# Performance work log

Hardware: AMD Instinct MI355X
Metric: run time of the kernel (lower is better)

Reference implementation:

```python
import jax, jax.numpy as jnp
import numpy as np

BN_EPS = 1e-5
LEAKY_SLOPE = 0.1


def conv_bn_leaky(x, w, gamma, beta, mean, var, pad):
    # Conv2d(no bias) + BatchNorm2d(inference) + LeakyReLU(0.1), NCHW/OIHW
    y = jax.lax.conv_general_dilated(
        x, w, window_strides=(1, 1), padding=[(pad, pad), (pad, pad)],
        dimension_numbers=("NCHW", "OIHW", "NCHW"))
    scale = gamma / jnp.sqrt(var + BN_EPS)
    shift = beta - mean * scale
    y = y * scale[None, :, None, None] + shift[None, :, None, None]
    return jnp.where(y > 0, y, LEAKY_SLOPE * y)


def reorg(x, s=2):
    # vedanet Reorg: out[b, (a*s+d)*C + c, i, j] = x[b, c, i*s+a, j*s+d]
    B, C, H, W = x.shape
    Ho, Wo = H // s, W // s
    return x.reshape(B, C, Ho, s, Wo, s).transpose(0, 3, 5, 1, 2, 4).reshape(B, s * s * C, Ho, Wo)


def setup_inputs() -> dict:
    key = jax.random.key(0)
    ks = jax.random.split(key, 10)
    B, H, W = 32, 19, 19
    NC, NA = 20, 5
    return {
        "stage6": jax.random.normal(ks[0], (B, 1024, H, W), jnp.float32),
        "stage5": jax.random.normal(ks[1], (B, 512, 2 * H, 2 * W), jnp.float32),
        "w1": jax.random.normal(ks[2], (64, 512, 1, 1), jnp.float32) * 0.05,
        "g1": jnp.ones((64,), jnp.float32),
        "b1": jnp.zeros((64,), jnp.float32),
        "m1": jax.random.normal(ks[3], (64,), jnp.float32) * 0.1,
        "v1": jax.random.uniform(ks[4], (64,), jnp.float32, 0.5, 1.5),
        "w2": jax.random.normal(ks[5], (1024, 1280, 3, 3), jnp.float32) * 0.02,
        "g2": jnp.ones((1024,), jnp.float32),
        "b2": jnp.zeros((1024,), jnp.float32),
        "m2": jax.random.normal(ks[6], (1024,), jnp.float32) * 0.1,
        "v2": jax.random.uniform(ks[7], (1024,), jnp.float32, 0.5, 1.5),
        "meta_state": jax.random.normal(ks[8], (NC, NA * 6, 1025), jnp.float32) * 0.05,
    }


def reference(stage6, stage5, w1, g1, b1, m1, v1, w2, g2, b2, m2, v2, meta_state):
    # layers[0]: 1x1 conv-bn-leaky on stage5, then Reorg(2) -> (B, 256, H, W)
    x = conv_bn_leaky(stage5, w1, g1, b1, m1, v1, pad=0)
    x = reorg(x, 2)
    # layers[1]: 3x3 conv-bn-leaky on concat -> (B, 1024, H, W)
    pre = conv_bn_leaky(jnp.concatenate([x, stage6], axis=1), w2, g2, b2, m2, v2, pad=1)
    # meta_predict: per-class 1x1 conv, batched as one einsum
    cls_w = meta_state[:, :, :-1]   # (NC, NA*6, 1024)
    cls_b = meta_state[:, :, -1]    # (NC, NA*6)
    out = jnp.einsum("bkij,cmk->bcmij", pre, cls_w) + cls_b[None, :, :, None, None]
    B, NC, M = pre.shape[0], meta_state.shape[0], meta_state.shape[1]
    return out.reshape(B * NC, M, pre.shape[2], pre.shape[3])
```

## Files before the change

kernel.cpp:

```cpp
#include <hip/hip_runtime.h>

typedef unsigned short u16;
typedef unsigned int   u32;

typedef __attribute__((ext_vector_type(8))) short bf16x8;
typedef __attribute__((ext_vector_type(4))) float f32x4;

__device__ __forceinline__ u16 f2bf(float f) {
  u32 u = __float_as_uint(f);
  u32 r = (u + 0x7fffu + ((u >> 16) & 1u)) >> 16;
  return (u16)r;
}

__device__ __forceinline__ void async16(const void* g, void* l) {
  __builtin_amdgcn_global_load_lds(
      (const __attribute__((address_space(1))) u32*)g,
      (__attribute__((address_space(3))) u32*)l, 16, 0, 0);
}

__global__ __launch_bounds__(256) void mega_prep_kern(
    const float* __restrict__ stage5, const float* __restrict__ s6,
    const float* __restrict__ w1,
    const float* __restrict__ g1, const float* __restrict__ b1,
    const float* __restrict__ m1, const float* __restrict__ v1,
    const float* __restrict__ w2, const float* __restrict__ g2,
    const float* __restrict__ b2, const float* __restrict__ m2,
    const float* __restrict__ v2, const float* __restrict__ meta,
    u16* __restrict__ in_bf, u16* __restrict__ w2p,
    u16* __restrict__ clsp, float* __restrict__ clsb,
    float* __restrict__ shift2)
{
  __shared__ __align__(16) char smem[8704];
  const int bid = blockIdx.x;
  const int t = threadIdx.x;

  if (bid < 722) {
    float* sc_s = (float*)smem;
    float* sh_s = (float*)(smem + 256);
    char*  aT   = smem + 512;
    char*  bT   = smem + 4608;
    const int w = t >> 6, lane = t & 63;
    if (t < 64) {
      float s = g1[t] * rsqrtf(v1[t] + 1e-5f);
      sc_s[t] = s;
      sh_s[t] = b1[t] - m1[t] * s;
    }
    const int m0 = bid * 64;
    const int pS = t & 63, gS = t >> 6;
    const int mS = m0 + pS;
    const int bS = mS / 1444, hwS = mS - bS * 1444;
    const float* s5 = stage5 + (size_t)bS * (512 * 1444) + hwS;
    const int ocA = t >> 2, icqA = t & 3;
    const float* w1r = w1 + (size_t)ocA * 512 + icqA * 8;
    char* aW = aT + (ocA >> 4) * 1024 + (icqA * 16 + (ocA & 15)) * 16;
    char* bW = bT + pS * 64 + ((gS ^ ((pS >> 1) & 3))) * 16;
    const int bR = (w * 16 + (lane & 15)) * 64 +
                   (((lane >> 4) ^ (((lane & 15) >> 1) & 3))) * 16;
    f32x4 acc[4] = {};
    __syncthreads();
    const float sA = sc_s[ocA];
    for (int kc = 0; kc < 16; ++kc) {
      const int ic0 = kc * 32;
      float a8[8], b8[8];
#pragma unroll
      for (int e = 0; e < 8; ++e) a8[e] = w1r[ic0 + e];
#pragma unroll
      for (int e = 0; e < 8; ++e) b8[e] = s5[(size_t)(ic0 + gS * 8 + e) * 1444];
      __syncthreads();
      uint4 av, bv;
      av.x = (u32)f2bf(a8[0] * sA) | ((u32)f2bf(a8[1] * sA) << 16);
      av.y = (u32)f2bf(a8[2] * sA) | ((u32)f2bf(a8[3] * sA) << 16);
      av.z = (u32)f2bf(a8[4] * sA) | ((u32)f2bf(a8[5] * sA) << 16);
      av.w = (u32)f2bf(a8[6] * sA) | ((u32)f2bf(a8[7] * sA) << 16);
      bv.x = (u32)f2bf(b8[0]) | ((u32)f2bf(b8[1]) << 16);
      bv.y = (u32)f2bf(b8[2]) | ((u32)f2bf(b8[3]) << 16);
      bv.z = (u32)f2bf(b8[4]) | ((u32)f2bf(b8[5]) << 16);
      bv.w = (u32)f2bf(b8[6]) | ((u32)f2bf(b8[7]) << 16);
      *(uint4*)aW = av;
      *(uint4*)bW = bv;
      __syncthreads();
      bf16x8 bfv = *(const bf16x8*)(bT + bR);
#pragma unroll
      for (int i = 0; i < 4; ++i) {
        bf16x8 af = *(const bf16x8*)(aT + i * 1024 + lane * 16);
        acc[i] = __builtin_amdgcn_mfma_f32_16x16x32_bf16(af, bfv, acc[i], 0, 0, 0);
      }
    }
    const int mE = m0 + w * 16 + (lane & 15);
    const int bE = mE / 1444, hwE = mE - bE * 1444;
    const int h = hwE / 38, wq = hwE - h * 38;
    const int ho = h >> 1, wo = wq >> 1, q = ((h & 1) << 1) | (wq & 1);
    u16* dst = in_bf + (((size_t)bE * 21 + 1 + ho) * 21 + 1 + wo) * 1280 + q * 64;
    const int lq = lane >> 4;
#pragma unroll
    for (int i = 0; i < 4; ++i) {
      int oc = i * 16 + lq * 4;
      float v0 = acc[i][0] + sh_s[oc + 0]; v0 = v0 > 0.f ? v0 : 0.1f * v0;
      float v1_ = acc[i][1] + sh_s[oc + 1]; v1_ = v1_ > 0.f ? v1_ : 0.1f * v1_;
      float v2_ = acc[i][2] + sh_s[oc + 2]; v2_ = v2_ > 0.f ? v2_ : 0.1f * v2_;
      float v3 = acc[i][3] + sh_s[oc + 3]; v3 = v3 > 0.f ? v3 : 0.1f * v3;
      u32 lo = (u32)f2bf(v0) | ((u32)f2bf(v1_) << 16);
      u32 hi = (u32)f2bf(v2_) | ((u32)f2bf(v3) << 16);
      u32* dp = (u32*)(dst + oc);
      dp[0] = lo; dp[1] = hi;
    }
    return;
  }

  if (bid < 3794) {
    u16 (*tile)[66] = (u16(*)[66])smem;
    const int sub = bid - 722;
    const int jt = sub % 6, ct = (sub / 6) % 16, b = sub / 96;
    const int ij0 = jt * 64, c0 = ct * 64;
    const int col = t & 63, rr = t >> 6;
#pragma unroll
    for (int r = 0; r < 16; ++r) {
      int cl = r * 4 + rr;
      int ij = ij0 + col;
      float v = 0.f;
      if (ij < 361) v = s6[((size_t)b * 1024 + c0 + cl) * 361 + ij];
      tile[cl][col] = f2bf(v);
    }
    __syncthreads();
#pragma unroll
    for (int r = 0; r < 16; ++r) {
      int ijl = r * 4 + rr;
      int ij = ij0 + ijl;
      if (ij < 361) {
        int i = ij / 19, j = ij - i * 19;
        in_bf[(((size_t)b * 21 + 1 + i) * 21 + 1 + j) * 1280 + 256 + c0 + col] =
            tile[col][ijl];
      }
    }
    return;
  }

  if (bid < 5394) {
    int gi = (bid - 3794) * 256 + t;
    int b = gi / 12800;
    int rem = gi - b * 12800;
    int p = rem / 160, qq = rem - p * 160;
    int row, col;
    if (p < 21)      { row = 0;      col = p; }
    else if (p < 42) { row = 20;     col = p - 21; }
    else if (p < 61) { row = p - 41; col = 0; }
    else             { row = p - 60; col = 20; }
    uint4 z = {0u, 0u, 0u, 0u};
    *(uint4*)(in_bf + (((size_t)b * 21 + row) * 21 + col) * 1280 + qq * 8) = z;
    return;
  }

  if (bid < 7794) {
    int idx = (bid - 5394) * 256 + t;
    int cm = idx >> 10, k = idx & 1023;
    int tile_ = cm >> 7, g = (cm >> 4) & 7, mm = cm & 15;
    int kc = k >> 5, ksub = (k >> 3) & 3, e = k & 7;
    size_t dst = (((size_t)tile_ * 32 + kc) * 8 + g) * 512
                 + (size_t)(ksub * 16 + mm) * 8 + e;
    clsp[dst] = f2bf(meta[(size_t)cm * 1025 + k]);
    if (idx < 600) clsb[idx] = meta[(size_t)idx * 1025 + 1024];
    if (idx < 1024) {
      float sc = g2[idx] * rsqrtf(v2[idx] + 1e-5f);
      shift2[idx] = b2[idx] - m2[idx] * sc;
    }
    return;
  }

  {
    u16* tile = (u16*)smem;
    const int sub = bid - 7794;
    const int icb = sub % 10;
    const int oc = sub / 10;
    const int ic0 = icb * 128;
    const float sc = g2[oc] * rsqrtf(v2[oc] + 1e-5f);
    const float* src = w2 + (size_t)oc * 11520 + (size_t)ic0 * 9;
#pragma unroll
    for (int p = t; p < 1152; p += 256) {
      float v = src[p];
      int ic_l = p / 9;
      int khw = p - ic_l * 9;
      tile[khw * 130 + ic_l] = f2bf(v * sc);
    }
    __syncthreads();
    if (t < 144) {
      int khw = t >> 4, c = (t >> 2) & 3, ksub = t & 3;
      int kc = khw * 40 + icb * 4 + c;
      const u16* s = &tile[khw * 130 + c * 32 + ksub * 8];
      uint4 v;
      v.x = (u32)s[0] | ((u32)s[1] << 16);
      v.y = (u32)s[2] | ((u32)s[3] << 16);
      v.z = (u32)s[4] | ((u32)s[5] << 16);
      v.w = (u32)s[6] | ((u32)s[7] << 16);
      size_t dst = (((size_t)(oc >> 7) * 360 + kc) * 8 + ((oc >> 4) & 7)) * 512
                   + (size_t)(ksub * 16 + (oc & 15)) * 8;
      *(uint4*)(w2p + dst) = v;
    }
  }
}

__global__ __launch_bounds__(256) void conv2_gemm_kern(
    const u16* __restrict__ Wp, const u16* __restrict__ Ig,
    const float* __restrict__ shift2, u16* __restrict__ pre)
{
  __shared__ u16 Wa[128 * 32];
  __shared__ u16 Ib[128 * 32];
  __shared__ float shft[128];
  const int t = threadIdx.x;
  const int w = t >> 6, lane = t & 63;
  const int lin = blockIdx.x + 91 * blockIdx.y;
  const int m0 = (lin >> 3) * 128;
  const int oc0 = (lin & 7) * 128;

  if (t < 128) shft[t] = shift2[oc0 + t];

  const u16* pW0 = Wp + ((size_t)(oc0 >> 7) * 2880 + w) * 512 + lane * 8;

  const int rw = t >> 2;
  const int rpart = ((t & 3) ^ ((t >> 3) & 3)) * 8;
  int mA = m0 + rw;       if (mA > 11551) mA = 11551;
  int mB = m0 + 64 + rw;  if (mB > 11551) mB = 11551;
  int bA = mA / 361, ijA = mA - bA * 361;
  int ohA = ijA / 19, owA = ijA - ohA * 19;
  int bB = mB / 361, ijB = mB - bB * 361;
  int ohB = ijB / 19, owB = ijB - ohB * 19;
  const u16* pI0 = Ig + (size_t)((bA * 21 + ohA) * 21 + owA) * 1280 + rpart;
  const u16* pI1 = Ig + (size_t)((bB * 21 + ohB) * 21 + owB) * 1280 + rpart;

  u16* waS0 = &Wa[w * 512];
  u16* waS1 = &Wa[2048 + w * 512];
  u16* ibS0 = &Ib[w * 512];
  u16* ibS1 = &Ib[2048 + w * 512];

  const int aBase = (w >> 1) * 2048 + lane * 8;
  const int bBase = (w & 1) * 2048 + (lane & 15) * 32 +
                    (((lane >> 4) ^ ((lane >> 1) & 3))) * 8;

  f32x4 acc[4][4] = {};

  for (int khw = 0; khw < 9; ++khw) {
    const int kh = khw / 3, kw = khw - kh * 3;
    const size_t iOffB = (size_t)(kh * 21 + kw) * 1280;
    const size_t wOffB = (size_t)khw * 40 * 4096;
    for (int icc = 0; icc < 40; ++icc) {
      const size_t io = iOffB + (size_t)icc * 32;
      const size_t wo_ = wOffB + (size_t)icc * 4096;
      async16(pW0 + wo_, waS0);
      async16(pW0 + wo_ + 2048, waS1);
      async16(pI0 + io, ibS0);
      async16(pI1 + io, ibS1);
      __syncthreads();
      bf16x8 af[4], bfv[4];
#pragma unroll
      for (int i = 0; i < 4; ++i)
        af[i] = *(const bf16x8*)&Wa[aBase + i * 512];
#pragma unroll
      for (int j = 0; j < 4; ++j)
        bfv[j] = *(const bf16x8*)&Ib[bBase + j * 512];
#pragma unroll
      for (int i = 0; i < 4; ++i)
#pragma unroll
        for (int j = 0; j < 4; ++j)
          acc[i][j] = __builtin_amdgcn_mfma_f32_16x16x32_bf16(
              af[i], bfv[j], acc[i][j], 0, 0, 0);
      __syncthreads();
    }
  }

  const int aRow = (w >> 1) * 64, bRow = (w & 1) * 64;
  const int lq = lane >> 4, lr = lane & 15;
#pragma unroll
  for (int j = 0; j < 4; ++j) {
    int m = m0 + bRow + j * 16 + lr;
    if (m >= 11552) continue;
    u16* prow = pre + (size_t)m * 1024 + oc0;
#pragma unroll
    for (int i = 0; i < 4; ++i) {
      int ocl = aRow + i * 16 + lq * 4;
      float v0 = acc[i][j][0] + shft[ocl + 0]; v0 = v0 > 0.f ? v0 : 0.1f * v0;
      float v1 = acc[i][j][1] + shft[ocl + 1]; v1 = v1 > 0.f ? v1 : 0.1f * v1;
      float v2 = acc[i][j][2] + shft[ocl + 2]; v2 = v2 > 0.f ? v2 : 0.1f * v2;
      float v3 = acc[i][j][3] + shft[ocl + 3]; v3 = v3 > 0.f ? v3 : 0.1f * v3;
      u32 lo = (u32)f2bf(v0) | ((u32)f2bf(v1) << 16);
      u32 hi = (u32)f2bf(v2) | ((u32)f2bf(v3) << 16);
      u32* dp = (u32*)(prow + ocl);
      dp[0] = lo; dp[1] = hi;
    }
  }
}

__global__ __launch_bounds__(256) void einsum_gemm_kern(
    const u16* __restrict__ Ap, const u16* __restrict__ Bg,
    const float* __restrict__ biasg, float* __restrict__ out)
{
  __shared__ u16 Wa[128 * 32];
  __shared__ u16 Ib[128 * 32];
  __shared__ float sbias[128];
  const int t = threadIdx.x;
  const int w = t >> 6, lane = t & 63;
  const int m0 = blockIdx.x * 128;
  const int cm0 = blockIdx.y * 128;
  if (t < 128) { int c = cm0 + t; sbias[t] = (c < 600) ? biasg[c] : 0.f; }

  const u16* pA0 = Ap + ((size_t)(cm0 >> 7) * 256 + w) * 512 + lane * 8;

  const int rw = t >> 2;
  const int rpart = ((t & 3) ^ ((t >> 3) & 3)) * 8;
  int rB0 = m0 + rw;        if (rB0 > 11551) rB0 = 11551;
  int rB1 = m0 + 64 + rw;   if (rB1 > 11551) rB1 = 11551;
  const u16* pB0 = Bg + (size_t)rB0 * 1024 + rpart;
  const u16* pB1 = Bg + (size_t)rB1 * 1024 + rpart;

  u16* waS0 = &Wa[w * 512];
  u16* waS1 = &Wa[2048 + w * 512];
  u16* ibS0 = &Ib[w * 512];
  u16* ibS1 = &Ib[2048 + w * 512];

  const int aBase = (w >> 1) * 2048 + lane * 8;
  const int bBase = (w & 1) * 2048 + (lane & 15) * 32 +
                    (((lane >> 4) ^ ((lane >> 1) & 3))) * 8;

  f32x4 acc[4][4] = {};

  for (int kt = 0; kt < 32; ++kt) {
    const size_t off = (size_t)kt * 32;
    async16(pA0 + (size_t)kt * 4096, waS0);
    async16(pA0 + (size_t)kt * 4096 + 2048, waS1);
    async16(pB0 + off, ibS0);
    async16(pB1 + off, ibS1);
    __syncthreads();
    bf16x8 af[4], bfv[4];
#pragma unroll
    for (int i = 0; i < 4; ++i)
      af[i] = *(const bf16x8*)&Wa[aBase + i * 512];
#pragma unroll
    for (int j = 0; j < 4; ++j)
      bfv[j] = *(const bf16x8*)&Ib[bBase + j * 512];
#pragma unroll
    for (int i = 0; i < 4; ++i)
#pragma unroll
      for (int j = 0; j < 4; ++j)
        acc[i][j] = __builtin_amdgcn_mfma_f32_16x16x32_bf16(
            af[i], bfv[j], acc[i][j], 0, 0, 0);
    __syncthreads();
  }

  const int aRow = (w >> 1) * 64, bRow = (w & 1) * 64;
  const int lq = lane >> 4, lr = lane & 15;
#pragma unroll
  for (int j = 0; j < 4; ++j) {
    int m = m0 + bRow + j * 16 + lr;
    if (m >= 11552) continue;
    int b = m / 361, ij = m - b * 361;
    float* obase = out + (size_t)b * 216600 + ij;
#pragma unroll
    for (int i = 0; i < 4; ++i) {
      int cml = aRow + i * 16 + lq * 4;
#pragma unroll
      for (int r = 0; r < 4; ++r) {
        int cm = cm0 + cml + r;
        if (cm < 600) obase[(size_t)cm * 361] = acc[i][j][r] + sbias[cml + r];
      }
    }
  }
}

extern "C" void kernel_launch(void* const* d_in, const int* in_sizes, int n_in,
                              void* d_out, int out_size, void* d_ws, size_t ws_size,
                              hipStream_t stream)
{
  const float* stage6 = (const float*)d_in[0];
  const float* stage5 = (const float*)d_in[1];
  const float* w1 = (const float*)d_in[2];
  const float* g1 = (const float*)d_in[3];
  const float* b1 = (const float*)d_in[4];
  const float* m1 = (const float*)d_in[5];
  const float* v1 = (const float*)d_in[6];
  const float* w2 = (const float*)d_in[7];
  const float* g2 = (const float*)d_in[8];
  const float* b2 = (const float*)d_in[9];
  const float* m2 = (const float*)d_in[10];
  const float* v2 = (const float*)d_in[11];
  const float* meta = (const float*)d_in[12];
  float* out = (float*)d_out;

  char* ws = (char*)d_ws;
  u16*   in_bf  = (u16*)(ws);
  u16*   w2p    = (u16*)(ws + 36126720);
  u16*   prebf  = (u16*)(ws + 59719680);
  u16*   clsp   = (u16*)(ws + 83378176);
  float* clsb   = (float*)(ws + 84688896);
  float* shift2 = (float*)(ws + 84691456);

  mega_prep_kern<<<18034, 256, 0, stream>>>(
      stage5, stage6, w1, g1, b1, m1, v1, w2, g2, b2, m2, v2, meta,
      in_bf, w2p, clsp, clsb, shift2);
  conv2_gemm_kern<<<dim3(91, 8), 256, 0, stream>>>(w2p, in_bf, shift2, prebf);
  einsum_gemm_kern<<<dim3(91, 5), 256, 0, stream>>>(clsp, prebf, clsb, out);
}
```

Baseline: 602.8 us.

## Rewrite conv2 GEMM with 256x256 tiles, 4-stage async LDS pipeline, 512 threads

The implicit-GEMM conv kernel now computes 256x256 output tiles with 512-thread blocks, and the weight packing layout changes to match. Loads use a 4-deep ring of LDS buffers with async global-to-LDS copies issued three stages ahead, and explicit waitcnt, barriers and setprio interleave loads with MFMA. The aim is to hide global memory latency, raise data reuse per tile, and make tile order L2-friendly through the swizzled block mapping. The trade-off is far more LDS (about 128KB) and more accumulator registers, which limits occupancy, plus the risk of hand-written synchronisation bugs.

Result: no change. 591.8 us (-1.8%).

```diff
diff --git a/kernel.cpp b/kernel.cpp
--- a/kernel.cpp
+++ b/kernel.cpp
@@ -184,102 +184,141 @@
     __syncthreads();
     if (t < 144) {
       int khw = t >> 4, c = (t >> 2) & 3, ksub = t & 3;
-      int kc = khw * 40 + icb * 4 + c;
+      int kt = khw * 40 + icb * 4 + c;
       const u16* s = &tile[khw * 130 + c * 32 + ksub * 8];
       uint4 v;
       v.x = (u32)s[0] | ((u32)s[1] << 16);
       v.y = (u32)s[2] | ((u32)s[3] << 16);
       v.z = (u32)s[4] | ((u32)s[5] << 16);
       v.w = (u32)s[6] | ((u32)s[7] << 16);
-      size_t dst = (((size_t)(oc >> 7) * 360 + kc) * 8 + ((oc >> 4) & 7)) * 512
-                   + (size_t)(ksub * 16 + (oc & 15)) * 8;
+      int oc_l = oc & 255;
+      size_t dst = (((size_t)(oc >> 8) * 360 + kt) * 2 + (oc_l >> 7)) * 4096
+                   + (size_t)(((oc_l >> 4) & 7) * 64 + ksub * 16 + (oc & 15)) * 8;
       *(uint4*)(w2p + dst) = v;
     }
   }
 }
 
-__global__ __launch_bounds__(256) void conv2_gemm_kern(
+__global__ __launch_bounds__(512, 2) void conv2_gemm_kern(
     const u16* __restrict__ Wp, const u16* __restrict__ Ig,
     const float* __restrict__ shift2, u16* __restrict__ pre)
 {
-  __shared__ u16 Wa[128 * 32];
-  __shared__ u16 Ib[128 * 32];
-  __shared__ float shft[128];
+  __shared__ u16 As[4][8192];
+  __shared__ u16 Bs[4][8192];
+  __shared__ float shft[256];
+
   const int t = threadIdx.x;
   const int w = t >> 6, lane = t & 63;
-  const int lin = blockIdx.x + 91 * blockIdx.y;
-  const int m0 = (lin >> 3) * 128;
-  const int oc0 = (lin & 7) * 128;
-
-  if (t < 128) shft[t] = shift2[oc0 + t];
-
-  const u16* pW0 = Wp + ((size_t)(oc0 >> 7) * 2880 + w) * 512 + lane * 8;
+  const int wm = w >> 2, wn = w & 3;
+
+  const int s = ((blockIdx.x & 7) * 23) + (blockIdx.x >> 3);
+  const int mTile = s >> 2, ocTile = s & 3;
+  const int m0 = mTile * 256, oc0 = ocTile * 256;
 
   const int rw = t >> 2;
   const int rpart = ((t & 3) ^ ((t >> 3) & 3)) * 8;
-  int mA = m0 + rw;       if (mA > 11551) mA = 11551;
-  int mB = m0 + 64 + rw;  if (mB > 11551) mB = 11551;
-  int bA = mA / 361, ijA = mA - bA * 361;
-  int ohA = ijA / 19, owA = ijA - ohA * 19;
-  int bB = mB / 361, ijB = mB - bB * 361;
-  int ohB = ijB / 19, owB = ijB - ohB * 19;
+  int mA = m0 + rw;        if (mA > 11551) mA = 11551;
+  int mB = m0 + 128 + rw;  if (mB > 11551) mB = 11551;
+  const int bA = mA / 361, ijA = mA - bA * 361;
+  const int ohA = ijA / 19, owA = ijA - ohA * 19;
+  const int bB = mB / 361, ijB = mB - bB * 361;
+  const int ohB = ijB / 19, owB = ijB - ohB * 19;
   const u16* pI0 = Ig + (size_t)((bA * 21 + ohA) * 21 + owA) * 1280 + rpart;
   const u16* pI1 = Ig + (size_t)((bB * 21 + ohB) * 21 + owB) * 1280 + rpart;
 
-  u16* waS0 = &Wa[w * 512];
-  u16* waS1 = &Wa[2048 + w * 512];
-  u16* ibS0 = &Ib[w * 512];
-  u16* ibS1 = &Ib[2048 + w * 512];
-
-  const int aBase = (w >> 1) * 2048 + lane * 8;
-  const int bBase = (w & 1) * 2048 + (lane & 15) * 32 +
-                    (((lane >> 4) ^ ((lane >> 1) & 3))) * 8;
-
-  f32x4 acc[4][4] = {};
-
-  for (int khw = 0; khw < 9; ++khw) {
-    const int kh = khw / 3, kw = khw - kh * 3;
-    const size_t iOffB = (size_t)(kh * 21 + kw) * 1280;
-    const size_t wOffB = (size_t)khw * 40 * 4096;
-    for (int icc = 0; icc < 40; ++icc) {
-      const size_t io = iOffB + (size_t)icc * 32;
-      const size_t wo_ = wOffB + (size_t)icc * 4096;
-      async16(pW0 + wo_, waS0);
-      async16(pW0 + wo_ + 2048, waS1);
-      async16(pI0 + io, ibS0);
-      async16(pI1 + io, ibS1);
-      __syncthreads();
-      bf16x8 af[4], bfv[4];
-#pragma unroll
-      for (int i = 0; i < 4; ++i)
-        af[i] = *(const bf16x8*)&Wa[aBase + i * 512];
+  const u16* pW = Wp + (size_t)ocTile * 2949120 + (size_t)t * 8;
+
+  const int aOff = wm * 4096 + lane * 8;
+  const int bOff = (wn * 64 + (lane & 15)) * 32 +
+                   (((lane >> 4) ^ ((lane >> 1) & 3)) * 8);
+
+  int skh = 0, skw = 0, sicb = 0, sIo = 0;
+
+#pragma unroll
+  for (int st = 0; st < 3; ++st) {
+    async16(pW + (size_t)st * 8192,        &As[st][t * 8]);
+    async16(pI0 + sIo,                     &Bs[st][t * 8]);
+    async16(pW + (size_t)st * 8192 + 4096, &As[st][4096 + t * 8]);
+    async16(pI1 + sIo,                     &Bs[st][4096 + t * 8]);
+    ++sicb; sIo += 32;
+    if (sicb == 40) { sicb = 0; ++skw; if (skw == 3) { skw = 0; ++skh; }
+                      sIo = (skh * 21 + skw) * 1280; }
+  }
+  asm volatile("s_waitcnt vmcnt(8)" ::: "memory");
+  __builtin_amdgcn_s_barrier();
+
+  f32x4 acc[8][4] = {};
+
+  for (int kt = 0; kt < 360; ++kt) {
+    const int cb = kt & 3;
+    const u16* Ab = As[cb];
+    const u16* Bb = Bs[cb];
+    const int stb = (kt + 3) & 3;
+    const int st = (kt > 356) ? 359 : kt + 3;
+    const size_t aSrc = (size_t)st * 8192;
+
+    bf16x8 af[4], bfv[4];
+#pragma unroll
+    for (int i = 0; i < 4; ++i)
+      af[i] = *(const bf16x8*)&Ab[aOff + i * 512];
+#pragma unroll
+    for (int j = 0; j < 4; ++j)
+      bfv[j] = *(const bf16x8*)&Bb[bOff + j * 512];
+    async16(pW + aSrc, &As[stb][t * 8]);
+    async16(pI0 + sIo, &Bs[stb][t * 8]);
+    __builtin_amdgcn_s_barrier();
+    asm volatile("s_waitcnt lgkmcnt(0)" ::: "memory");
+    __builtin_amdgcn_sched_barrier(0);
+    __builtin_amdgcn_s_setprio(1);
+#pragma unroll
+    for (int i = 0; i < 4; ++i)
 #pragma unroll
       for (int j = 0; j < 4; ++j)
-        bfv[j] = *(const bf16x8*)&Ib[bBase + j * 512];
-#pragma unroll
-      for (int i = 0; i < 4; ++i)
-#pragma unroll
-        for (int j = 0; j < 4; ++j)
-          acc[i][j] = __builtin_amdgcn_mfma_f32_16x16x32_bf16(
-              af[i], bfv[j], acc[i][j], 0, 0, 0);
-      __syncthreads();
-    }
-  }
-
-  const int aRow = (w >> 1) * 64, bRow = (w & 1) * 64;
+        acc[i][j] = __builtin_amdgcn_mfma_f32_16x16x32_bf16(
+            af[i], bfv[j], acc[i][j], 0, 0, 0);
+    __builtin_amdgcn_s_setprio(0);
+    __builtin_amdgcn_s_barrier();
+
+#pragma unroll
+    for (int i = 0; i < 4; ++i)
+      af[i] = *(const bf16x8*)&Ab[aOff + 2048 + i * 512];
+    async16(pW + aSrc + 4096, &As[stb][4096 + t * 8]);
+    async16(pI1 + sIo,        &Bs[stb][4096 + t * 8]);
+    __builtin_amdgcn_s_barrier();
+    asm volatile("s_waitcnt lgkmcnt(0)" ::: "memory");
+    __builtin_amdgcn_sched_barrier(0);
+    __builtin_amdgcn_s_setprio(1);
+#pragma unroll
+    for (int i = 0; i < 4; ++i)
+#pragma unroll
+      for (int j = 0; j < 4; ++j)
+        acc[4 + i][j] = __builtin_amdgcn_mfma_f32_16x16x32_bf16(
+            af[i], bfv[j], acc[4 + i][j], 0, 0, 0);
+    __builtin_amdgcn_s_setprio(0);
+    asm volatile("s_waitcnt vmcnt(8)" ::: "memory");
+    __builtin_amdgcn_s_barrier();
+
+    ++sicb; sIo += 32;
+    if (sicb == 40) { sicb = 0; ++skw; if (skw == 3) { skw = 0; ++skh; }
+                      sIo = (skh * 21 + skw) * 1280; }
+  }
+
+  if (t < 256) shft[t] = shift2[oc0 + t];
+  __syncthreads();
+
   const int lq = lane >> 4, lr = lane & 15;
 #pragma unroll
   for (int j = 0; j < 4; ++j) {
-    int m = m0 + bRow + j * 16 + lr;
+    const int m = m0 + wn * 64 + j * 16 + lr;
     if (m >= 11552) continue;
-    u16* prow = pre + (size_t)m * 1024 + oc0;
-#pragma unroll
-    for (int i = 0; i < 4; ++i) {
-      int ocl = aRow + i * 16 + lq * 4;
-      float v0 = acc[i][j][0] + shft[ocl + 0]; v0 = v0 > 0.f ? v0 : 0.1f * v0;
-      float v1 = acc[i][j][1] + shft[ocl + 1]; v1 = v1 > 0.f ? v1 : 0.1f * v1;
-      float v2 = acc[i][j][2] + shft[ocl + 2]; v2 = v2 > 0.f ? v2 : 0.1f * v2;
-      float v3 = acc[i][j][3] + shft[ocl + 3]; v3 = v3 > 0.f ? v3 : 0.1f * v3;
+    u16* prow = pre + (size_t)m * 1024 + oc0 + wm * 128;
+#pragma unroll
+    for (int i = 0; i < 8; ++i) {
+      const int ocl = i * 16 + lq * 4;
+      float v0 = acc[i][j][0] + shft[wm * 128 + ocl + 0]; v0 = v0 > 0.f ? v0 : 0.1f * v0;
+      float v1 = acc[i][j][1] + shft[wm * 128 + ocl + 1]; v1 = v1 > 0.f ? v1 : 0.1f * v1;
+      float v2 = acc[i][j][2] + shft[wm * 128 + ocl + 2]; v2 = v2 > 0.f ? v2 : 0.1f * v2;
+      float v3 = acc[i][j][3] + shft[wm * 128 + ocl + 3]; v3 = v3 > 0.f ? v3 : 0.1f * v3;
       u32 lo = (u32)f2bf(v0) | ((u32)f2bf(v1) << 16);
       u32 hi = (u32)f2bf(v2) | ((u32)f2bf(v3) << 16);
       u32* dp = (u32*)(prow + ocl);
@@ -394,6 +433,6 @@
   mega_prep_kern<<<18034, 256, 0, stream>>>(
       stage5, stage6, w1, g1, b1, m1, v1, w2, g2, b2, m2, v2, meta,
       in_bf, w2p, clsp, clsb, shift2);
-  conv2_gemm_kern<<<dim3(91, 8), 256, 0, stream>>>(w2p, in_bf, shift2, prebf);
+  conv2_gemm_kern<<<184, 512, 0, stream>>>(w2p, in_bf, shift2, prebf);
   einsum_gemm_kern<<<dim3(91, 5), 256, 0, stream>>>(clsp, prebf, clsb, out);
 }
```
